# Performance work log

Hardware: AMD Instinct MI355X
Metric: run time of the kernel (lower is better)

## Reference

```python
import jax, jax.numpy as jnp
import numpy as np

B, DIM, H, W = 8, 512, 32, 32
HC, WC = 32, 32
NH, DH = 8, 64
DE = NH * DH  # dim_embed = 512


def setup_inputs() -> dict:
    key = jax.random.key(0)
    ks = jax.random.split(key, 6)
    return {
        "x": jax.random.normal(ks[0], (B, DIM, H, W), jnp.float32),
        "context": jax.random.normal(ks[1], (B, DIM, HC, WC), jnp.float32),
        "gamma": jnp.ones((DIM, 1, 1), jnp.float32),
        "w_q": jax.random.normal(ks[2], (DE, DIM), jnp.float32) * 0.02,
        "w_k": jax.random.normal(ks[3], (DE, DIM), jnp.float32) * 0.02,
        "w_v": jax.random.normal(ks[4], (DE, DIM), jnp.float32) * 0.02,
        "w_proj": jax.random.normal(ks[5], (DIM, DE), jnp.float32) * 0.02,
    }


def _rms_norm(t, gamma, scale):
    # torch F.normalize(dim=1): x / max(||x||_2, 1e-12) along channel axis
    nrm = jnp.sqrt(jnp.sum(t * t, axis=1, keepdims=True))
    return t / jnp.maximum(nrm, 1e-12) * scale * gamma


def _split_heads(t, h, w):
    # 'b (c n) h w -> (b n) (h w) c' with c=DH, n=NH
    b = t.shape[0]
    t = t.reshape(b, DH, NH, h, w).transpose(0, 2, 3, 4, 1)  # b n h w c
    return t.reshape(b * NH, h * w, DH)


def reference(x, context, gamma, w_q, w_k, w_v, w_proj):
    scale = float(DIM) ** 0.5
    xn = _rms_norm(x, gamma, scale)
    # faithful to source bug: self.norm (not norm_context) applied to context
    cn = _rms_norm(context, gamma, scale)

    q = jnp.einsum('bchw,oc->bohw', xn, w_q)
    k = jnp.einsum('bchw,oc->bohw', cn, w_k)
    v = jnp.einsum('bchw,oc->bohw', cn, w_v)

    q = _split_heads(q, H, W)      # (B*NH, H*W, DH)
    k = _split_heads(k, HC, WC)    # (B*NH, HC*WC, DH)
    v = _split_heads(v, HC, WC)

    qk = jnp.einsum('bmc,bnc->bmn', q, k) * (float(DH) ** -0.5)
    attn = jnp.einsum('bmn,bnc->bmc', jax.nn.softmax(qk, axis=-1) + 1e-8, v) + 1e-8

    # '(b n) (h w) c -> b (c n) h w'
    attn = attn.reshape(B, NH, H, W, DH).transpose(0, 4, 1, 2, 3).reshape(B, DE, H, W)
    return jnp.einsum('bchw,oc->bohw', attn, w_proj)
```

## Files before the change

### kernel.cpp

```cpp
#include <hip/hip_runtime.h>
#include <hip/hip_bf16.h>


typedef _Float16 half8v __attribute__((ext_vector_type(8)));
typedef __fp16 fp16x2 __attribute__((ext_vector_type(2)));
typedef __attribute__((ext_vector_type(4))) float float4v;
typedef __attribute__((ext_vector_type(16))) float float16v;
typedef __attribute__((ext_vector_type(2))) int int2v;

__device__ inline ushort f2h(float f) {
  union { _Float16 h; ushort u; } cv;
  cv.h = (_Float16)f;
  return cv.u;
}

__device__ inline void stage16(const void* g, void* l) {
  __builtin_amdgcn_global_load_lds(
      (const __attribute__((address_space(1))) unsigned*)g,
      (__attribute__((address_space(3))) unsigned*)l, 16, 0, 0);
}

__device__ inline void permswap(unsigned& a, unsigned& b) {
#if __has_builtin(__builtin_amdgcn_permlane32_swap)
  int2v r = __builtin_amdgcn_permlane32_swap((int)a, (int)b, false, false);
  a = (unsigned)r[0];
  b = (unsigned)r[1];
#else
  unsigned pa = (unsigned)__shfl_xor((int)a, 32, 64);
  unsigned pb = (unsigned)__shfl_xor((int)b, 32, 64);
  bool hb = (threadIdx.x & 32) != 0;
  unsigned na = hb ? pb : a;
  unsigned nb = hb ? b : pa;
  a = na;
  b = nb;
#endif
}

__global__ __launch_bounds__(256) void prep_kernel(
    const float* __restrict__ x, const float* __restrict__ ctx,
    const float* __restrict__ wq, const float* __restrict__ wk,
    const float* __restrict__ wv, const float* __restrict__ wp,
    const float* __restrict__ gamma, ushort* __restrict__ xT,
    ushort* __restrict__ cT, float* __restrict__ sx, float* __restrict__ sc,
    ushort* __restrict__ wf) {
  __shared__ ushort tile[32 * 512];
  __shared__ float part[32][32];
  const int bid = blockIdx.x;
  const int t = threadIdx.x;

  if (bid < 512) {
    const int tensor = bid >> 8;
    const int b = (bid >> 5) & 7;
    const int pos0 = (bid & 31) << 5;
    const float* src = tensor ? ctx : x;
    ushort* dstT = tensor ? cT : xT;
    float* dstS = tensor ? sc : sx;
    unsigned* tile32 = (unsigned*)tile;

    const int pcq = t & 7;
    const int crg = t >> 3;
    float ssq[4] = {0.f, 0.f, 0.f, 0.f};

    const float* srcb = src + ((size_t)b * 512) * 1024 + pos0;
    for (int p = 0; p < 8; ++p) {
      const int cr0 = p * 64 + crg * 2;
      float4 v0 = *(const float4*)&srcb[(size_t)cr0 * 1024 + pcq * 4];
      float4 v1 = *(const float4*)&srcb[(size_t)(cr0 + 1) * 1024 + pcq * 4];
      ssq[0] += v0.x * v0.x + v1.x * v1.x;
      ssq[1] += v0.y * v0.y + v1.y * v1.y;
      ssq[2] += v0.z * v0.z + v1.z * v1.z;
      ssq[3] += v0.w * v0.w + v1.w * v1.w;
      const int cp = cr0 >> 1;
      float e0[4] = {v0.x, v0.y, v0.z, v0.w};
      float e1[4] = {v1.x, v1.y, v1.z, v1.w};
#pragma unroll
      for (int j = 0; j < 4; ++j) {
        const int posl = pcq * 4 + j;
        unsigned pk = (unsigned)f2h(e0[j]) | ((unsigned)f2h(e1[j]) << 16);
        tile32[posl * 256 + (cp ^ posl)] = pk;
      }
    }
#pragma unroll
    for (int j = 0; j < 4; ++j) part[crg][pcq * 4 + j] = ssq[j];
    __syncthreads();
    if (t < 32) {
      float s = 0.f;
#pragma unroll
      for (int g2 = 0; g2 < 32; ++g2) s += part[g2][t];
      dstS[b * 1024 + pos0 + t] =
          22.627416997969522f / fmaxf(sqrtf(s), 1e-12f);
    }
    ushort* ob = dstT + ((size_t)b * 1024 + pos0) * 512;
#pragma unroll
    for (int ii = 0; ii < 8; ++ii) {
      const int m = t + ii * 256;
      const int posl = m >> 6, c16 = m & 63;
      uint4 u;
      u.x = tile32[posl * 256 + ((c16 * 4 + 0) ^ posl)];
      u.y = tile32[posl * 256 + ((c16 * 4 + 1) ^ posl)];
      u.z = tile32[posl * 256 + ((c16 * 4 + 2) ^ posl)];
      u.w = tile32[posl * 256 + ((c16 * 4 + 3) ^ posl)];
      *(uint4*)&ob[(size_t)posl * 512 + c16 * 8] = u;
    }
  } else {
    const int wbid = bid - 512;
    const int m = wbid >> 7;
    const float* W = (m == 0) ? wq : (m == 1) ? wk : (m == 2) ? wv : wp;
    const int r = (wbid & 127) * 4 + (t >> 6);
    const int c8 = (t & 63) * 8;
    ushort h[8];
    if (m < 3) {
      const int o = ((r & 63) << 3) + (r >> 6);
      const float* wr_ = &W[(size_t)o * 512 + c8];
#pragma unroll
      for (int j = 0; j < 8; ++j) h[j] = f2h(wr_[j] * gamma[c8 + j]);
    } else {
#pragma unroll
      for (int j = 0; j < 8; ++j) {
        const int cc = c8 + j;
        const int cs = ((cc & 63) << 3) + (cc >> 6);
        h[j] = f2h(W[(size_t)r * 512 + cs]);
      }
    }
    ushort* dst = &wf[((size_t)m * 512 + r) * 512 + c8];
    uint4 u;
    u.x = (unsigned)h[0] | ((unsigned)h[1] << 16);
    u.y = (unsigned)h[2] | ((unsigned)h[3] << 16);
    u.z = (unsigned)h[4] | ((unsigned)h[5] << 16);
    u.w = (unsigned)h[6] | ((unsigned)h[7] << 16);
    *(uint4*)dst = u;
  }
}

__global__ __launch_bounds__(256, 2) void qkv_kernel(
    const ushort* __restrict__ xT, const ushort* __restrict__ cT,
    const ushort* __restrict__ wf, const float* __restrict__ sx,
    const float* __restrict__ sc, ushort* __restrict__ qh,
    ushort* __restrict__ kh, ushort* __restrict__ vt) {
  const int z = blockIdx.z;
  const int proj = z % 3;
  const int b = z / 3;
  const ushort* XT = (proj == 0) ? xT : cT;
  const float* S = (proj == 0) ? sx : sc;
  const ushort* WF = wf + (size_t)proj * 262144;
  const int pos0 = blockIdx.x << 7;
  const int o0 = blockIdx.y << 7;

  __shared__ __align__(16) unsigned char lds[65536];
  unsigned char* Al = lds;
  unsigned char* Bl = lds + 32768;

  const int t = threadIdx.x, w = t >> 6, lane = t & 63;
  const int g = lane >> 4, l15 = lane & 15;
  const int wr = w >> 1, wc = w & 1;
  const int srow_ = lane >> 3;
  const int sslot16 = ((lane & 7) ^ srow_) << 4;

  const unsigned char* Asrc =
      (const unsigned char*)(XT + ((size_t)b * 1024 + pos0) * 512);
  const unsigned char* Bsrc = (const unsigned char*)(WF + (size_t)o0 * 512);

#define QSTAGE(buf, kk)                                                     \
  do {                                                                      \
    _Pragma("unroll") for (int i = 0; i < 4; ++i) {                         \
      const int j = (w << 2) + i;                                           \
      stage16(Asrc + (size_t)((j << 3) + srow_) * 1024 + (kk)*128 + sslot16,\
              Al + (buf)*16384 + (j << 10));                                \
      stage16(Bsrc + (size_t)((j << 3) + srow_) * 1024 + (kk)*128 + sslot16,\
              Bl + (buf)*16384 + (j << 10));                                \
    }                                                                       \
  } while (0)

  float4v acc[4][4];
#pragma unroll
  for (int i = 0; i < 4; ++i)
#pragma unroll
    for (int j2 = 0; j2 < 4; ++j2) acc[i][j2] = (float4v){0.f, 0.f, 0.f, 0.f};

  QSTAGE(0, 0);
  __syncthreads();

  for (int kk = 0; kk < 8; ++kk) {
    const int cur = kk & 1;
    if (kk < 7) QSTAGE(cur ^ 1, kk + 1);
    const unsigned char* At = Al + cur * 16384;
    const unsigned char* Bt = Bl + cur * 16384;
    half8v af[4][2], bf[4][2];
#pragma unroll
    for (int mt = 0; mt < 4; ++mt) {
      const int row = (wr << 6) + (mt << 4) + l15;
      const unsigned char* rb = At + row * 128;
      af[mt][0] = *(const half8v*)(rb + (((g) ^ (row & 7)) << 4));
      af[mt][1] = *(const half8v*)(rb + (((4 + g) ^ (row & 7)) << 4));
    }
#pragma unroll
    for (int nt = 0; nt < 4; ++nt) {
      const int row = (wc << 6) + (nt << 4) + l15;
      const unsigned char* rb = Bt + row * 128;
      bf[nt][0] = *(const half8v*)(rb + (((g) ^ (row & 7)) << 4));
      bf[nt][1] = *(const half8v*)(rb + (((4 + g) ^ (row & 7)) << 4));
    }
    if (proj < 2) {
#pragma unroll
      for (int mt = 0; mt < 4; ++mt)
#pragma unroll
        for (int nt = 0; nt < 4; ++nt) {
          acc[mt][nt] = __builtin_amdgcn_mfma_f32_16x16x32_f16(
              af[mt][0], bf[nt][0], acc[mt][nt], 0, 0, 0);
          acc[mt][nt] = __builtin_amdgcn_mfma_f32_16x16x32_f16(
              af[mt][1], bf[nt][1], acc[mt][nt], 0, 0, 0);
        }
    } else {
#pragma unroll
      for (int mt = 0; mt < 4; ++mt)
#pragma unroll
        for (int nt = 0; nt < 4; ++nt) {
          acc[mt][nt] = __builtin_amdgcn_mfma_f32_16x16x32_f16(
              bf[nt][0], af[mt][0], acc[mt][nt], 0, 0, 0);
          acc[mt][nt] = __builtin_amdgcn_mfma_f32_16x16x32_f16(
              bf[nt][1], af[mt][1], acc[mt][nt], 0, 0, 0);
        }
    }
    __syncthreads();
  }
#undef QSTAGE

  if (proj < 2) {
    ushort* Out = (proj == 0) ? qh : kh;
    const float qsc = (proj == 0) ? 0.125f : 1.0f;
#pragma unroll
    for (int mt = 0; mt < 4; ++mt) {
      const int posb = pos0 + (wr << 6) + (mt << 4) + (g << 2);
      float4 sv4 = *(const float4*)&S[b * 1024 + posb];
      float sarr[4] = {sv4.x * qsc, sv4.y * qsc, sv4.z * qsc, sv4.w * qsc};
#pragma unroll
      for (int nt = 0; nt < 4; ++nt) {
        const int oo = o0 + (wc << 6) + (nt << 4) + l15;
#pragma unroll
        for (int r = 0; r < 4; ++r) {
          float val = acc[mt][nt][r] * sarr[r];
          Out[((size_t)(b * 1024 + posb + r)) * 512 + oo] = f2h(val);
        }
      }
    }
  } else {
#pragma unroll
    for (int mt = 0; mt < 4; ++mt) {
      const int pos = pos0 + (wr << 6) + (mt << 4) + l15;
      const float sval = S[b * 1024 + pos];
#pragma unroll
      for (int nt = 0; nt < 4; ++nt) {
        const int ob = o0 + (wc << 6) + (nt << 4) + (g << 2);
#pragma unroll
        for (int r = 0; r < 4; ++r) {
          const int oo = ob + r;
          vt[((size_t)(b * 512 + oo)) * 1024 + pos] = f2h(acc[mt][nt][r] * sval);
        }
      }
    }
  }
}

__global__ __launch_bounds__(512, 2) void attn_kernel(
    const ushort* __restrict__ qh, const ushort* __restrict__ kh,
    const ushort* __restrict__ vt, ushort* __restrict__ am) {
  __shared__ __align__(16) unsigned char lds[32768];

  const int bh = blockIdx.y;
  const int b = bh >> 3, n = bh & 7;
  const int mbase = blockIdx.x << 8;
  const int t = threadIdx.x;
  const int w = t >> 6;
  const int lane = t & 63;
  const int l31 = lane & 31;
  const int hi = lane >> 5;
  const int swz = (l31 & 7) << 4;

  half8v qf[4];
  const size_t qrow = (size_t)b * 1024 + mbase + w * 32 + l31;
#pragma unroll
  for (int kc = 0; kc < 4; ++kc)
    qf[kc] = *(const half8v*)(qh + qrow * 512 + n * 64 + kc * 16 + hi * 8);

  float16v o[2];
#pragma unroll
  for (int d2 = 0; d2 < 2; ++d2)
#pragma unroll
    for (int e = 0; e < 16; ++e) o[d2][e] = 0.f;
  float rsum = 0.f;

  const unsigned char* kgb =
      (const unsigned char*)kh + (size_t)b * 1048576 + n * 128;
  const unsigned char* vgb =
      (const unsigned char*)vt + (size_t)b * 1048576 + n * 131072;
  const int kro = (t >> 3) * 1024 + (((t & 7) ^ ((t >> 3) & 7)) << 4);
  const int vro = (t >> 3) * 2048 + (((t & 7) ^ ((t >> 3) & 7)) << 4);

#define ASTAGE(buf, kt)                                                   \
  do {                                                                    \
    stage16(kgb + (size_t)(kt)*65536 + kro, lds + (buf)*8192 + t * 16);   \
    stage16(vgb + (size_t)(kt)*128 + vro,                                 \
            lds + 16384 + (buf)*8192 + t * 16);                           \
  } while (0)

  ASTAGE(0, 0);
  __syncthreads();

  for (int kt = 0; kt < 16; ++kt) {
    const int cur = kt & 1;
    if (kt < 15) ASTAGE(cur ^ 1, kt + 1);
    const unsigned char* Kc = lds + cur * 8192;
    const unsigned char* Vc = lds + 16384 + cur * 8192;

    half8v vf[4][2];
#pragma unroll
    for (int ks = 0; ks < 4; ++ks)
#pragma unroll
      for (int d2 = 0; d2 < 2; ++d2)
        vf[ks][d2] = *(const half8v*)(Vc + (l31 + 32 * d2) * 128 +
                                      ((hi * 16 + ks * 32) ^ swz));

#pragma unroll
    for (int kt2 = 0; kt2 < 2; ++kt2) {
      half8v kf[4];
#pragma unroll
      for (int kc = 0; kc < 4; ++kc)
        kf[kc] = *(const half8v*)(Kc + (l31 + 32 * kt2) * 128 +
                                  ((hi * 16 + kc * 32) ^ swz));
      float16v st;
#pragma unroll
      for (int e = 0; e < 16; ++e) st[e] = 0.f;
#pragma unroll
      for (int kc = 0; kc < 4; ++kc)
        st = __builtin_amdgcn_mfma_f32_32x32x16_f16(kf[kc], qf[kc], st, 0, 0,
                                                    0);
      float p[16];
#pragma unroll
      for (int r = 0; r < 16; ++r) p[r] = __expf(st[r]);
      rsum += (((p[0] + p[1]) + (p[2] + p[3])) +
               ((p[4] + p[5]) + (p[6] + p[7]))) +
              (((p[8] + p[9]) + (p[10] + p[11])) +
               ((p[12] + p[13]) + (p[14] + p[15])));
      unsigned wds[8];
#pragma unroll
      for (int j = 0; j < 8; ++j) {
        union { fp16x2 h; unsigned u; } cv_;
        cv_.h = __builtin_amdgcn_cvt_pkrtz(p[2 * j], p[2 * j + 1]);
        wds[j] = cv_.u;
      }
      permswap(wds[0], wds[2]);
      permswap(wds[1], wds[3]);
      permswap(wds[4], wds[6]);
      permswap(wds[5], wds[7]);
      union { half8v h; unsigned u[4]; } pf0, pf1;
      pf0.u[0] = wds[0]; pf0.u[1] = wds[1];
      pf0.u[2] = wds[2]; pf0.u[3] = wds[3];
      pf1.u[0] = wds[4]; pf1.u[1] = wds[5];
      pf1.u[2] = wds[6]; pf1.u[3] = wds[7];
#pragma unroll
      for (int d2 = 0; d2 < 2; ++d2) {
        o[d2] = __builtin_amdgcn_mfma_f32_32x32x16_f16(
            pf0.h, vf[kt2 * 2 + 0][d2], o[d2], 0, 0, 0);
        o[d2] = __builtin_amdgcn_mfma_f32_32x32x16_f16(
            pf1.h, vf[kt2 * 2 + 1][d2], o[d2], 0, 0, 0);
      }
    }
    __syncthreads();
  }
#undef ASTAGE

  const float inv = 1.0f / (rsum + __shfl_xor(rsum, 32, 64));

#pragma unroll
  for (int r = 0; r < 16; ++r) {
    const int qloc = (r & 3) + 8 * (r >> 2) + 4 * hi;
    const float iv = __shfl(inv, qloc, 64);
    const size_t rowbase =
        ((size_t)(b * 1024 + mbase + w * 32 + qloc)) * 512 + n * 64 + l31;
#pragma unroll
    for (int d2 = 0; d2 < 2; ++d2) {
      am[rowbase + 32 * d2] = f2h(o[d2][r] * iv);
    }
  }
}

__global__ __launch_bounds__(256, 3) void proj_kernel(
    const ushort* __restrict__ am, const ushort* __restrict__ wf3,
    float* __restrict__ out) {
  const int b = blockIdx.z;
  const int pos0 = blockIdx.x << 7;
  const int o0 = blockIdx.y << 6;

  __shared__ __align__(16) unsigned char lds[49152];
  unsigned char* Al = lds;
  unsigned char* Bl = lds + 16384;

  const int t = threadIdx.x, w = t >> 6, lane = t & 63;
  const int g = lane >> 4, l15 = lane & 15;
  const int wr = w >> 1, wc = w & 1;

  const unsigned char* Asrc = (const unsigned char*)(wf3 + (size_t)o0 * 512);
  const unsigned char* Bsrc =
      (const unsigned char*)(am + ((size_t)b * 1024 + pos0) * 512);

#define PSTAGE(buf, kk)                                                      \
  do {                                                                       \
    _Pragma("unroll") for (int i = 0; i < 2; ++i) {                          \
      const int u = t + (i << 8);                                            \
      const int row = u >> 3;                                                \
      stage16(Asrc + (size_t)row * 1024 + (kk)*128 +                         \
                  (((u & 7) ^ (row & 7)) << 4),                              \
              Al + (buf)*8192 + u * 16);                                     \
    }                                                                        \
    _Pragma("unroll") for (int i = 0; i < 4; ++i) {                          \
      const int u = t + (i << 8);                                            \
      const int row = u >> 3;                                                \
      stage16(Bsrc + (size_t)row * 1024 + (kk)*128 +                         \
                  (((u & 7) ^ (row & 7)) << 4),                              \
              Bl + (buf)*16384 + u * 16);                                    \
    }                                                                        \
  } while (0)

  float4v acc[2][4];
#pragma unroll
  for (int i = 0; i < 2; ++i)
#pragma unroll
    for (int j2 = 0; j2 < 4; ++j2) acc[i][j2] = (float4v){0.f, 0.f, 0.f, 0.f};

  PSTAGE(0, 0);
  __syncthreads();

  for (int kk = 0; kk < 8; ++kk) {
    const int cur = kk & 1;
    if (kk < 7) PSTAGE(cur ^ 1, kk + 1);
    const unsigned char* At = Al + cur * 8192;
    const unsigned char* Bt = Bl + cur * 16384;
    half8v af[2][2], bf[4][2];
#pragma unroll
    for (int mt = 0; mt < 2; ++mt) {
      const int row = (wr << 5) + (mt << 4) + l15;
      const unsigned char* rb = At + row * 128;
      af[mt][0] = *(const half8v*)(rb + (((g) ^ (row & 7)) << 4));
      af[mt][1] = *(const half8v*)(rb + (((4 + g) ^ (row & 7)) << 4));
    }
#pragma unroll
    for (int nt = 0; nt < 4; ++nt) {
      const int row = (wc << 6) + (nt << 4) + l15;
      const unsigned char* rb = Bt + row * 128;
      bf[nt][0] = *(const half8v*)(rb + (((g) ^ (row & 7)) << 4));
      bf[nt][1] = *(const half8v*)(rb + (((4 + g) ^ (row & 7)) << 4));
    }
#pragma unroll
    for (int mt = 0; mt < 2; ++mt)
#pragma unroll
      for (int nt = 0; nt < 4; ++nt) {
        acc[mt][nt] = __builtin_amdgcn_mfma_f32_16x16x32_f16(
            af[mt][0], bf[nt][0], acc[mt][nt], 0, 0, 0);
        acc[mt][nt] = __builtin_amdgcn_mfma_f32_16x16x32_f16(
            af[mt][1], bf[nt][1], acc[mt][nt], 0, 0, 0);
      }
    __syncthreads();
  }
#undef PSTAGE

#pragma unroll
  for (int mt = 0; mt < 2; ++mt) {
    const int ob = o0 + (wr << 5) + (mt << 4) + (g << 2);
#pragma unroll
    for (int nt = 0; nt < 4; ++nt) {
      const int pos = pos0 + (wc << 6) + (nt << 4) + l15;
#pragma unroll
      for (int r = 0; r < 4; ++r) {
        out[((size_t)(b * 512 + ob + r)) * 1024 + pos] = acc[mt][nt][r];
      }
    }
  }
}

extern "C" void kernel_launch(void* const* d_in, const int* in_sizes, int n_in,
                              void* d_out, int out_size, void* d_ws,
                              size_t ws_size, hipStream_t stream) {
  const float* x = (const float*)d_in[0];
  const float* ctx = (const float*)d_in[1];
  const float* gamma = (const float*)d_in[2];
  const float* wq = (const float*)d_in[3];
  const float* wk = (const float*)d_in[4];
  const float* wv = (const float*)d_in[5];
  const float* wp = (const float*)d_in[6];
  float* out = (float*)d_out;

  char* ws = (char*)d_ws;
  float* sx = (float*)(ws);
  float* sc = (float*)(ws + 32768);
  ushort* xT = (ushort*)(ws + 65536);
  ushort* cT = (ushort*)(ws + 65536 + 8388608);
  ushort* wf = (ushort*)(ws + 65536 + 16777216);
  ushort* qh = (ushort*)(ws + 65536 + 18874368);
  ushort* kh = (ushort*)(ws + 65536 + 27262976);
  ushort* vt = (ushort*)(ws + 65536 + 35651584);
  ushort* am = xT;

  prep_kernel<<<1024, 256, 0, stream>>>(x, ctx, wq, wk, wv, wp, gamma, xT, cT,
                                        sx, sc, wf);
  qkv_kernel<<<dim3(8, 4, 24), 256, 0, stream>>>(xT, cT, wf, sx, sc, qh, kh,
                                                 vt);
  attn_kernel<<<dim3(4, 64), 512, 0, stream>>>(qh, kh, vt, am);
  proj_kernel<<<dim3(8, 8, 8), 256, 0, stream>>>(am, wf + 3 * 262144, out);
}
```

Before: 63.58 us.

## Fuse RMS norm and fp16 transpose into QKV GEMM reading fp32 inputs directly

```diff
diff --git a/kernel.cpp b/kernel.cpp
--- a/kernel.cpp
+++ b/kernel.cpp
@@ -11,6 +11,12 @@
 __device__ inline ushort f2h(float f) {
   union { _Float16 h; ushort u; } cv;
   cv.h = (_Float16)f;
+  return cv.u;
+}
+
+__device__ inline unsigned pk2(float a, float b) {
+  union { fp16x2 h; unsigned u; } cv;
+  cv.h = __builtin_amdgcn_cvt_pkrtz(a, b);
   return cv.u;
 }
 
@@ -36,227 +42,156 @@
 #endif
 }
 
-__global__ __launch_bounds__(256) void prep_kernel(
-    const float* __restrict__ x, const float* __restrict__ ctx,
+__global__ __launch_bounds__(256) void wconv_kernel(
     const float* __restrict__ wq, const float* __restrict__ wk,
     const float* __restrict__ wv, const float* __restrict__ wp,
-    const float* __restrict__ gamma, ushort* __restrict__ xT,
-    ushort* __restrict__ cT, float* __restrict__ sx, float* __restrict__ sc,
-    ushort* __restrict__ wf) {
-  __shared__ ushort tile[32 * 512];
-  __shared__ float part[32][32];
-  const int bid = blockIdx.x;
+    const float* __restrict__ gamma, ushort* __restrict__ wf) {
+  const int wbid = blockIdx.x;
   const int t = threadIdx.x;
-
-  if (bid < 512) {
-    const int tensor = bid >> 8;
-    const int b = (bid >> 5) & 7;
-    const int pos0 = (bid & 31) << 5;
-    const float* src = tensor ? ctx : x;
-    ushort* dstT = tensor ? cT : xT;
-    float* dstS = tensor ? sc : sx;
-    unsigned* tile32 = (unsigned*)tile;
-
-    const int pcq = t & 7;
-    const int crg = t >> 3;
-    float ssq[4] = {0.f, 0.f, 0.f, 0.f};
-
-    const float* srcb = src + ((size_t)b * 512) * 1024 + pos0;
-    for (int p = 0; p < 8; ++p) {
-      const int cr0 = p * 64 + crg * 2;
-      float4 v0 = *(const float4*)&srcb[(size_t)cr0 * 1024 + pcq * 4];
-      float4 v1 = *(const float4*)&srcb[(size_t)(cr0 + 1) * 1024 + pcq * 4];
-      ssq[0] += v0.x * v0.x + v1.x * v1.x;
-      ssq[1] += v0.y * v0.y + v1.y * v1.y;
-      ssq[2] += v0.z * v0.z + v1.z * v1.z;
-      ssq[3] += v0.w * v0.w + v1.w * v1.w;
-      const int cp = cr0 >> 1;
-      float e0[4] = {v0.x, v0.y, v0.z, v0.w};
-      float e1[4] = {v1.x, v1.y, v1.z, v1.w};
-#pragma unroll
-      for (int j = 0; j < 4; ++j) {
-        const int posl = pcq * 4 + j;
-        unsigned pk = (unsigned)f2h(e0[j]) | ((unsigned)f2h(e1[j]) << 16);
-        tile32[posl * 256 + (cp ^ posl)] = pk;
-      }
-    }
-#pragma unroll
-    for (int j = 0; j < 4; ++j) part[crg][pcq * 4 + j] = ssq[j];
-    __syncthreads();
-    if (t < 32) {
-      float s = 0.f;
-#pragma unroll
-      for (int g2 = 0; g2 < 32; ++g2) s += part[g2][t];
-      dstS[b * 1024 + pos0 + t] =
-          22.627416997969522f / fmaxf(sqrtf(s), 1e-12f);
-    }
-    ushort* ob = dstT + ((size_t)b * 1024 + pos0) * 512;
-#pragma unroll
-    for (int ii = 0; ii < 8; ++ii) {
-      const int m = t + ii * 256;
-      const int posl = m >> 6, c16 = m & 63;
-      uint4 u;
-      u.x = tile32[posl * 256 + ((c16 * 4 + 0) ^ posl)];
-      u.y = tile32[posl * 256 + ((c16 * 4 + 1) ^ posl)];
-      u.z = tile32[posl * 256 + ((c16 * 4 + 2) ^ posl)];
-      u.w = tile32[posl * 256 + ((c16 * 4 + 3) ^ posl)];
-      *(uint4*)&ob[(size_t)posl * 512 + c16 * 8] = u;
-    }
+  const int m = wbid >> 7;
+  const float* W = (m == 0) ? wq : (m == 1) ? wk : (m == 2) ? wv : wp;
+  const int r = (wbid & 127) * 4 + (t >> 6);
+  const int c8 = (t & 63) * 8;
+  ushort h[8];
+  if (m < 3) {
+    const int o = ((r & 63) << 3) + (r >> 6);
+    const float* wr_ = &W[(size_t)o * 512 + c8];
+#pragma unroll
+    for (int j = 0; j < 8; ++j) h[j] = f2h(wr_[j] * gamma[c8 + j]);
   } else {
-    const int wbid = bid - 512;
-    const int m = wbid >> 7;
-    const float* W = (m == 0) ? wq : (m == 1) ? wk : (m == 2) ? wv : wp;
-    const int r = (wbid & 127) * 4 + (t >> 6);
-    const int c8 = (t & 63) * 8;
-    ushort h[8];
-    if (m < 3) {
-      const int o = ((r & 63) << 3) + (r >> 6);
-      const float* wr_ = &W[(size_t)o * 512 + c8];
-#pragma unroll
-      for (int j = 0; j < 8; ++j) h[j] = f2h(wr_[j] * gamma[c8 + j]);
-    } else {
-#pragma unroll
-      for (int j = 0; j < 8; ++j) {
-        const int cc = c8 + j;
-        const int cs = ((cc & 63) << 3) + (cc >> 6);
-        h[j] = f2h(W[(size_t)r * 512 + cs]);
-      }
-    }
-    ushort* dst = &wf[((size_t)m * 512 + r) * 512 + c8];
-    uint4 u;
-    u.x = (unsigned)h[0] | ((unsigned)h[1] << 16);
-    u.y = (unsigned)h[2] | ((unsigned)h[3] << 16);
-    u.z = (unsigned)h[4] | ((unsigned)h[5] << 16);
-    u.w = (unsigned)h[6] | ((unsigned)h[7] << 16);
-    *(uint4*)dst = u;
-  }
+#pragma unroll
+    for (int j = 0; j < 8; ++j) {
+      const int cc = c8 + j;
+      const int cs = ((cc & 63) << 3) + (cc >> 6);
+      h[j] = f2h(W[(size_t)r * 512 + cs]);
+    }
+  }
+  ushort* dst = &wf[((size_t)m * 512 + r) * 512 + c8];
+  uint4 u;
+  u.x = (unsigned)h[0] | ((unsigned)h[1] << 16);
+  u.y = (unsigned)h[2] | ((unsigned)h[3] << 16);
+  u.z = (unsigned)h[4] | ((unsigned)h[5] << 16);
+  u.w = (unsigned)h[6] | ((unsigned)h[7] << 16);
+  *(uint4*)dst = u;
 }
 
 __global__ __launch_bounds__(256, 2) void qkv_kernel(
-    const ushort* __restrict__ xT, const ushort* __restrict__ cT,
-    const ushort* __restrict__ wf, const float* __restrict__ sx,
-    const float* __restrict__ sc, ushort* __restrict__ qh,
+    const float* __restrict__ x, const float* __restrict__ ctx,
+    const ushort* __restrict__ wf, ushort* __restrict__ qh,
     ushort* __restrict__ kh, ushort* __restrict__ vt) {
+  __shared__ __align__(16) unsigned char lds[32768];
   const int z = blockIdx.z;
-  const int proj = z % 3;
-  const int b = z / 3;
-  const ushort* XT = (proj == 0) ? xT : cT;
-  const float* S = (proj == 0) ? sx : sc;
+  const int proj = z % 3, b = z / 3;
+  const float* X = (proj == 0) ? x : ctx;
   const ushort* WF = wf + (size_t)proj * 262144;
-  const int pos0 = blockIdx.x << 7;
-  const int o0 = blockIdx.y << 7;
-
-  __shared__ __align__(16) unsigned char lds[65536];
-  unsigned char* Al = lds;
-  unsigned char* Bl = lds + 32768;
-
+  const int pos0 = blockIdx.x << 7, o0 = blockIdx.y << 7;
   const int t = threadIdx.x, w = t >> 6, lane = t & 63;
   const int g = lane >> 4, l15 = lane & 15;
   const int wr = w >> 1, wc = w & 1;
-  const int srow_ = lane >> 3;
-  const int sslot16 = ((lane & 7) ^ srow_) << 4;
-
-  const unsigned char* Asrc =
-      (const unsigned char*)(XT + ((size_t)b * 1024 + pos0) * 512);
-  const unsigned char* Bsrc = (const unsigned char*)(WF + (size_t)o0 * 512);
-
-#define QSTAGE(buf, kk)                                                     \
-  do {                                                                      \
-    _Pragma("unroll") for (int i = 0; i < 4; ++i) {                         \
-      const int j = (w << 2) + i;                                           \
-      stage16(Asrc + (size_t)((j << 3) + srow_) * 1024 + (kk)*128 + sslot16,\
-              Al + (buf)*16384 + (j << 10));                                \
-      stage16(Bsrc + (size_t)((j << 3) + srow_) * 1024 + (kk)*128 + sslot16,\
-              Bl + (buf)*16384 + (j << 10));                                \
-    }                                                                       \
-  } while (0)
+
+  const float* xb =
+      X + (size_t)b * 524288 + (size_t)(g * 8) * 1024 + pos0 + wc * 64 + l15;
+  const ushort* wb = WF + (size_t)(o0 + wr * 64 + l15) * 512 + g * 8;
 
   float4v acc[4][4];
 #pragma unroll
   for (int i = 0; i < 4; ++i)
 #pragma unroll
-    for (int j2 = 0; j2 < 4; ++j2) acc[i][j2] = (float4v){0.f, 0.f, 0.f, 0.f};
-
-  QSTAGE(0, 0);
-  __syncthreads();
-
-  for (int kk = 0; kk < 8; ++kk) {
-    const int cur = kk & 1;
-    if (kk < 7) QSTAGE(cur ^ 1, kk + 1);
-    const unsigned char* At = Al + cur * 16384;
-    const unsigned char* Bt = Bl + cur * 16384;
-    half8v af[4][2], bf[4][2];
+    for (int j = 0; j < 4; ++j) acc[i][j] = (float4v){0.f, 0.f, 0.f, 0.f};
+  float ssq[4] = {0.f, 0.f, 0.f, 0.f};
+
+#pragma unroll
+  for (int k = 0; k < 8; ++k) {
+    half8v af[4][2];
+#pragma unroll
+    for (int mt = 0; mt < 4; ++mt)
+#pragma unroll
+      for (int kc = 0; kc < 2; ++kc)
+        af[mt][kc] =
+            *(const half8v*)(wb + (size_t)mt * 8192 + k * 64 + kc * 32);
+    half8v bf[4][2];
+#pragma unroll
+    for (int nt = 0; nt < 4; ++nt) {
+#pragma unroll
+      for (int kc = 0; kc < 2; ++kc) {
+        float v0 = xb[(size_t)(k * 64 + kc * 32 + 0) * 1024 + nt * 16];
+        float v1 = xb[(size_t)(k * 64 + kc * 32 + 1) * 1024 + nt * 16];
+        float v2 = xb[(size_t)(k * 64 + kc * 32 + 2) * 1024 + nt * 16];
+        float v3 = xb[(size_t)(k * 64 + kc * 32 + 3) * 1024 + nt * 16];
+        float v4 = xb[(size_t)(k * 64 + kc * 32 + 4) * 1024 + nt * 16];
+        float v5 = xb[(size_t)(k * 64 + kc * 32 + 5) * 1024 + nt * 16];
+        float v6 = xb[(size_t)(k * 64 + kc * 32 + 6) * 1024 + nt * 16];
+        float v7 = xb[(size_t)(k * 64 + kc * 32 + 7) * 1024 + nt * 16];
+        ssq[nt] += v0 * v0 + v1 * v1 + v2 * v2 + v3 * v3 + v4 * v4 +
+                   v5 * v5 + v6 * v6 + v7 * v7;
+        union { half8v h; unsigned u[4]; } pk;
+        pk.u[0] = pk2(v0, v1);
+        pk.u[1] = pk2(v2, v3);
+        pk.u[2] = pk2(v4, v5);
+        pk.u[3] = pk2(v6, v7);
+        bf[nt][kc] = pk.h;
+      }
+    }
+#pragma unroll
+    for (int mt = 0; mt < 4; ++mt)
+#pragma unroll
+      for (int nt = 0; nt < 4; ++nt) {
+        acc[mt][nt] = __builtin_amdgcn_mfma_f32_16x16x32_f16(
+            af[mt][0], bf[nt][0], acc[mt][nt], 0, 0, 0);
+        acc[mt][nt] = __builtin_amdgcn_mfma_f32_16x16x32_f16(
+            af[mt][1], bf[nt][1], acc[mt][nt], 0, 0, 0);
+      }
+  }
+
+  float s[4];
+#pragma unroll
+  for (int nt = 0; nt < 4; ++nt) {
+    float r = ssq[nt] + __shfl_xor(ssq[nt], 16, 64);
+    r += __shfl_xor(r, 32, 64);
+    s[nt] = 22.627416997969522f / fmaxf(sqrtf(r), 1e-12f);
+  }
+  if (proj == 0) {
+#pragma unroll
+    for (int nt = 0; nt < 4; ++nt) s[nt] *= 0.125f;
+  }
+
+  if (proj == 2) {
 #pragma unroll
     for (int mt = 0; mt < 4; ++mt) {
-      const int row = (wr << 6) + (mt << 4) + l15;
-      const unsigned char* rb = At + row * 128;
-      af[mt][0] = *(const half8v*)(rb + (((g) ^ (row & 7)) << 4));
-      af[mt][1] = *(const half8v*)(rb + (((4 + g) ^ (row & 7)) << 4));
-    }
-#pragma unroll
-    for (int nt = 0; nt < 4; ++nt) {
-      const int row = (wc << 6) + (nt << 4) + l15;
-      const unsigned char* rb = Bt + row * 128;
-      bf[nt][0] = *(const half8v*)(rb + (((g) ^ (row & 7)) << 4));
-      bf[nt][1] = *(const half8v*)(rb + (((4 + g) ^ (row & 7)) << 4));
-    }
-    if (proj < 2) {
-#pragma unroll
-      for (int mt = 0; mt < 4; ++mt)
-#pragma unroll
-        for (int nt = 0; nt < 4; ++nt) {
-          acc[mt][nt] = __builtin_amdgcn_mfma_f32_16x16x32_f16(
-              af[mt][0], bf[nt][0], acc[mt][nt], 0, 0, 0);
-          acc[mt][nt] = __builtin_amdgcn_mfma_f32_16x16x32_f16(
-              af[mt][1], bf[nt][1], acc[mt][nt], 0, 0, 0);
+#pragma unroll
+      for (int nt = 0; nt < 4; ++nt) {
+        const int pos = pos0 + wc * 64 + nt * 16 + l15;
+#pragma unroll
+        for (int r = 0; r < 4; ++r) {
+          const int oo = o0 + wr * 64 + mt * 16 + g * 4 + r;
+          vt[((size_t)(b * 512 + oo)) * 1024 + pos] =
+              f2h(acc[mt][nt][r] * s[nt]);
         }
-    } else {
-#pragma unroll
-      for (int mt = 0; mt < 4; ++mt)
-#pragma unroll
-        for (int nt = 0; nt < 4; ++nt) {
-          acc[mt][nt] = __builtin_amdgcn_mfma_f32_16x16x32_f16(
-              bf[nt][0], af[mt][0], acc[mt][nt], 0, 0, 0);
-          acc[mt][nt] = __builtin_amdgcn_mfma_f32_16x16x32_f16(
-              bf[nt][1], af[mt][1], acc[mt][nt], 0, 0, 0);
-        }
+      }
+    }
+  } else {
+#pragma unroll
+    for (int mt = 0; mt < 4; ++mt) {
+#pragma unroll
+      for (int nt = 0; nt < 4; ++nt) {
+        const int posl = wc * 64 + nt * 16 + l15;
+        const int slot = wr * 8 + mt * 2 + (g >> 1);
+        unsigned lo = pk2(acc[mt][nt][0] * s[nt], acc[mt][nt][1] * s[nt]);
+        unsigned hi2 = pk2(acc[mt][nt][2] * s[nt], acc[mt][nt][3] * s[nt]);
+        unsigned long long d = (unsigned long long)hi2 << 32 | lo;
+        *(unsigned long long*)(lds + posl * 256 +
+                               ((slot ^ (posl & 7)) << 4) + (g & 1) * 8) = d;
+      }
     }
     __syncthreads();
-  }
-#undef QSTAGE
-
-  if (proj < 2) {
     ushort* Out = (proj == 0) ? qh : kh;
-    const float qsc = (proj == 0) ? 0.125f : 1.0f;
-#pragma unroll
-    for (int mt = 0; mt < 4; ++mt) {
-      const int posb = pos0 + (wr << 6) + (mt << 4) + (g << 2);
-      float4 sv4 = *(const float4*)&S[b * 1024 + posb];
-      float sarr[4] = {sv4.x * qsc, sv4.y * qsc, sv4.z * qsc, sv4.w * qsc};
-#pragma unroll
-      for (int nt = 0; nt < 4; ++nt) {
-        const int oo = o0 + (wc << 6) + (nt << 4) + l15;
-#pragma unroll
-        for (int r = 0; r < 4; ++r) {
-          float val = acc[mt][nt][r] * sarr[r];
-          Out[((size_t)(b * 1024 + posb + r)) * 512 + oo] = f2h(val);
-        }
-      }
-    }
-  } else {
-#pragma unroll
-    for (int mt = 0; mt < 4; ++mt) {
-      const int pos = pos0 + (wr << 6) + (mt << 4) + l15;
-      const float sval = S[b * 1024 + pos];
-#pragma unroll
-      for (int nt = 0; nt < 4; ++nt) {
-        const int ob = o0 + (wc << 6) + (nt << 4) + (g << 2);
-#pragma unroll
-        for (int r = 0; r < 4; ++r) {
-          const int oo = ob + r;
-          vt[((size_t)(b * 512 + oo)) * 1024 + pos] = f2h(acc[mt][nt][r] * sval);
-        }
-      }
+    const int row = t >> 1, half = t & 1;
+#pragma unroll
+    for (int i = 0; i < 8; ++i) {
+      const int slot = half * 8 + i;
+      uint4 d = *(const uint4*)(lds + row * 256 + ((slot ^ (row & 7)) << 4));
+      *(uint4*)(Out + ((size_t)(b * 1024 + pos0 + row)) * 512 + o0 +
+                slot * 8) = d;
     }
   }
 }
@@ -343,11 +278,7 @@
                ((p[12] + p[13]) + (p[14] + p[15])));
       unsigned wds[8];
 #pragma unroll
-      for (int j = 0; j < 8; ++j) {
-        union { fp16x2 h; unsigned u; } cv_;
-        cv_.h = __builtin_amdgcn_cvt_pkrtz(p[2 * j], p[2 * j + 1]);
-        wds[j] = cv_.u;
-      }
+      for (int j = 0; j < 8; ++j) wds[j] = pk2(p[2 * j], p[2 * j + 1]);
       permswap(wds[0], wds[2]);
       permswap(wds[1], wds[3]);
       permswap(wds[4], wds[6]);
@@ -490,20 +421,14 @@
   float* out = (float*)d_out;
 
   char* ws = (char*)d_ws;
-  float* sx = (float*)(ws);
-  float* sc = (float*)(ws + 32768);
-  ushort* xT = (ushort*)(ws + 65536);
-  ushort* cT = (ushort*)(ws + 65536 + 8388608);
-  ushort* wf = (ushort*)(ws + 65536 + 16777216);
-  ushort* qh = (ushort*)(ws + 65536 + 18874368);
-  ushort* kh = (ushort*)(ws + 65536 + 27262976);
-  ushort* vt = (ushort*)(ws + 65536 + 35651584);
-  ushort* am = xT;
-
-  prep_kernel<<<1024, 256, 0, stream>>>(x, ctx, wq, wk, wv, wp, gamma, xT, cT,
-                                        sx, sc, wf);
-  qkv_kernel<<<dim3(8, 4, 24), 256, 0, stream>>>(xT, cT, wf, sx, sc, qh, kh,
-                                                 vt);
+  ushort* wf = (ushort*)(ws);
+  ushort* qh = (ushort*)(ws + 2097152);
+  ushort* kh = (ushort*)(ws + 10485760);
+  ushort* vt = (ushort*)(ws + 18874368);
+  ushort* am = (ushort*)(ws + 27262976);
+
+  wconv_kernel<<<512, 256, 0, stream>>>(wq, wk, wv, wp, gamma, wf);
+  qkv_kernel<<<dim3(8, 4, 24), 256, 0, stream>>>(x, ctx, wf, qh, kh, vt);
   attn_kernel<<<dim3(4, 64), 512, 0, stream>>>(qh, kh, vt, am);
   proj_kernel<<<dim3(8, 8, 8), 256, 0, stream>>>(am, wf + 3 * 262144, out);
 }
```

Result: slower. 97.29 us (+53.0%).
